# Optimization experiments

Hardware: AMD Instinct MI355X
Metric: run time of the kernel (lower is better)

Reference implementation:

```python
import jax, jax.numpy as jnp
import numpy as np
from jax import lax

NUM_CLASSES = 19
BINS_NUM = 51
LOSS_WEIGHT = 1.0


def setup_inputs() -> dict:
    key = jax.random.key(0)
    k1, k2 = jax.random.split(key)
    feature = jax.random.normal(k1, (1, 256, 64, 64), dtype=jnp.float32)
    label = jax.random.randint(k2, (1, 1, 64, 64), 0, NUM_CLASSES).astype(jnp.int64)
    return {"feature": feature, "label": label}


def reference(feature, label):
    # feature: [1, D, H, W]; label: [1, 1, H, W] (same spatial size -> nearest resize is identity)
    D = feature.shape[1]
    C = NUM_CLASSES
    F = feature[0].reshape(D, -1).T            # [N, D] pixel feature vectors
    L = label[0, 0].reshape(-1).astype(jnp.int32)  # [N] class id per pixel

    counts = jax.ops.segment_sum(jnp.ones(L.shape, jnp.float32), L, num_segments=C)  # [C]
    sum_f = jax.ops.segment_sum(F, L, num_segments=C)        # [C, D]
    sum_f2 = jax.ops.segment_sum(F * F, L, num_segments=C)   # [C, D]
    has = counts > 0
    cnt = jnp.maximum(counts, 1.0)
    miu = sum_f / cnt[:, None]                                # first-iter: direct assignment (no EMA yet)
    moment2 = sum_f2 / cnt[:, None]
    var = jnp.maximum(moment2 - miu ** 2, 1e-12)
    # stats are computed via detached numpy in the original -> no grad
    miu = lax.stop_gradient(miu)
    var = lax.stop_gradient(var)
    var_sample = var / 25.0

    bins = jnp.linspace(-5.0, 5.0, BINS_NUM).astype(jnp.float32)  # [B]

    # target gaussian pdf per (class, feature-dim, bin): [C, D, B]
    inv_norm_t = 1.0 / jnp.sqrt(2.0 * jnp.pi * var)
    target = jnp.exp(-0.5 * (bins[None, None, :] - miu[:, :, None]) ** 2 / var[:, :, None]) * inv_norm_t[:, :, None]

    # sample KDE per pixel, scatter-added into its class: [N, D, B] -> [C, D, B]
    vs_p = var_sample[L]                                      # [N, D]
    inv_norm_s = 1.0 / jnp.sqrt(2.0 * jnp.pi * vs_p)          # [N, D]
    K = jnp.exp(-0.5 * (bins[None, None, :] - F[:, :, None]) ** 2 / vs_p[:, :, None]) * inv_norm_s[:, :, None]
    samp = jax.ops.segment_sum(K, L, num_segments=C)          # [C, D, B]

    samp_den = jnp.where(has[:, None], jnp.maximum(samp.sum(-1), 1e-30), 1.0)[:, :, None]
    tgt_den = jnp.where(has[:, None], jnp.maximum(target.sum(-1), 1e-30), 1.0)[:, :, None]
    hist = samp / samp_den
    target = target / tgt_den

    # smooth L1 (beta=1, mean reduction) per class
    diff = hist - target
    ad = jnp.abs(diff)
    sl1 = jnp.where(ad < 1.0, 0.5 * diff * diff, ad - 0.5).mean(axis=(1, 2))  # [C]

    active = has & (jnp.arange(C) > 0)
    active_num = jnp.sum(active.astype(jnp.float32))
    loss = jnp.sum(jnp.where(active, sl1, 0.0)) / (active_num + 1e-12)
    return (LOSS_WEIGHT * loss, feature)
```

## Files before the change

### kernel.cpp

```cpp
#include <hip/hip_runtime.h>

#define N_PIX 4096
#define N_D   256
#define N_C   19
#define N_B   51
#define N_BLOCKS_MAIN (18 * 64)

#define OFF_LIST   0
#define OFF_COUNTS 311296
#define OFF_ACC    311424
#define OFF_TICKET 311428

__global__ __launch_bounds__(256) void k_pre(const float* __restrict__ feature,
                                             const int* __restrict__ label,
                                             float* __restrict__ out,
                                             int* __restrict__ list,
                                             int* __restrict__ counts,
                                             float* __restrict__ acc,
                                             int* __restrict__ ticket) {
    const int b = blockIdx.x;
    if (b < N_C) {
        const int c = b;
        const int w = threadIdx.x >> 6;
        const int lane = threadIdx.x & 63;
        __shared__ int wcnt[4];
        if (c == 0 && threadIdx.x == 0) { *acc = 0.f; *ticket = 0; }

        const int q0 = w * 1024;
        int cnt = 0;
        for (int base = 0; base < 1024; base += 64) {
            cnt += (int)__popcll(__ballot(label[q0 + base + lane] == c));
        }
        if (lane == 0) wcnt[w] = cnt;
        __syncthreads();
        int m = 0;
#pragma unroll
        for (int i = 0; i < 4; ++i) m += (i < w) ? wcnt[i] : 0;

        for (int base = 0; base < 1024; base += 64) {
            const int n = q0 + base + lane;
            const bool match = (label[n] == c);
            const unsigned long long mask = __ballot(match);
            if (match) list[c * N_PIX + m + __popcll(mask & ((1ull << lane) - 1ull))] = n;
            m += (int)__popcll(mask);
        }
        if (w == 3 && lane == 0) counts[c] = m;
    } else {
        const int tid = (b - N_C) * 256 + threadIdx.x;
        const int nth = (256 - N_C) * 256;
        const float4* __restrict__ src = (const float4*)feature;
        float* __restrict__ dst = out + 1;
        for (int i = tid; i < N_PIX * N_D / 4; i += nth) {
            const float4 v = src[i];
            dst[4 * i + 0] = v.x;
            dst[4 * i + 1] = v.y;
            dst[4 * i + 2] = v.z;
            dst[4 * i + 3] = v.w;
        }
    }
}

__global__ __launch_bounds__(256) void k_main(const float* __restrict__ feature,
                                              const int* __restrict__ list,
                                              const int* __restrict__ counts,
                                              float* __restrict__ acc,
                                              int* __restrict__ ticket,
                                              float* __restrict__ out) {
    const int c = blockIdx.x + 1;
    const int w = threadIdx.x >> 6;
    const int d = blockIdx.y * 4 + w;
    const int lane = threadIdx.x & 63;
    const int m = counts[c];
    __shared__ float blk[4];
    float part = 0.f;
    if (m > 0) {
        const float* __restrict__ row = feature + d * N_PIX;
        const int* __restrict__ lst = list + c * N_PIX;

        float s1 = 0.f, s2 = 0.f;
        for (int j = lane; j < m; j += 64) {
            const float f = row[lst[j]];
            s1 += f;
            s2 += f * f;
        }
#pragma unroll
        for (int off = 32; off; off >>= 1) {
            s1 += __shfl_xor(s1, off);
            s2 += __shfl_xor(s2, off);
        }
        const float cnt = (float)m;
        const float mu = s1 / cnt;
        const float v = fmaxf(s2 / cnt - mu * mu, 1e-12f);

        const float LOG2E = 1.44269504088896340736f;
        const float as = -12.5f * LOG2E / v;
        const float at = -0.5f * LOG2E / v;
        const float bin = (lane < N_B) ? fmaf(0.2f, (float)lane, -5.0f) : 1e18f;
        const float tt = bin - mu;
        const float targ = __builtin_amdgcn_exp2f(at * tt * tt);

        float a0 = 0.f, a1 = 0.f, a2 = 0.f, a3 = 0.f;
        for (int base = 0; base < m; base += 64) {
            const int j = base + lane;
            const float fl = (j < m) ? row[lst[j]] : -1e18f;
#pragma unroll
            for (int k = 0; k < 64; k += 4) {
                const float f0 = __shfl(fl, k);
                const float f1 = __shfl(fl, k + 1);
                const float f2 = __shfl(fl, k + 2);
                const float f3 = __shfl(fl, k + 3);
                const float t0 = f0 - bin, t1 = f1 - bin, t2 = f2 - bin, t3 = f3 - bin;
                a0 += __builtin_amdgcn_exp2f(as * t0 * t0);
                a1 += __builtin_amdgcn_exp2f(as * t1 * t1);
                a2 += __builtin_amdgcn_exp2f(as * t2 * t2);
                a3 += __builtin_amdgcn_exp2f(as * t3 * t3);
            }
        }
        const float acc_s = (a0 + a1) + (a2 + a3);

        float ss = acc_s, st = targ;
#pragma unroll
        for (int off = 32; off; off >>= 1) {
            ss += __shfl_xor(ss, off);
            st += __shfl_xor(st, off);
        }
        const float hist = acc_s / fmaxf(ss, 1e-30f);
        const float tgt  = targ  / fmaxf(st, 1e-30f);
        const float diff = hist - tgt;
        const float ad = fabsf(diff);
        float sl1 = (ad < 1.f) ? 0.5f * diff * diff : ad - 0.5f;
#pragma unroll
        for (int off = 32; off; off >>= 1) sl1 += __shfl_down(sl1, off);
        part = sl1;
    }
    if (lane == 0) blk[w] = part;
    __syncthreads();
    if (threadIdx.x == 0) {
        atomicAdd(acc, blk[0] + blk[1] + blk[2] + blk[3]);
        __threadfence();
        const int t = atomicAdd(ticket, 1);
        if (t == N_BLOCKS_MAIN - 1) {
            int active = 0;
            for (int cc = 1; cc < N_C; ++cc) active += (counts[cc] > 0) ? 1 : 0;
            const float total = atomicAdd(acc, 0.0f);
            out[0] = total / (float)(N_D * N_B) / ((float)active + 1e-12f);
        }
    }
}

extern "C" void kernel_launch(void* const* d_in, const int* in_sizes, int n_in,
                              void* d_out, int out_size, void* d_ws, size_t ws_size,
                              hipStream_t stream) {
    const float* feature = (const float*)d_in[0];
    const int* label = (const int*)d_in[1];
    float* out = (float*)d_out;
    char* ws = (char*)d_ws;
    int* list = (int*)(ws + OFF_LIST);
    int* counts = (int*)(ws + OFF_COUNTS);
    float* acc = (float*)(ws + OFF_ACC);
    int* ticket = (int*)(ws + OFF_TICKET);

    k_pre<<<256, 256, 0, stream>>>(feature, label, out, list, counts, acc, ticket);
    dim3 grid(N_C - 1, N_D / 4);
    k_main<<<grid, 256, 0, stream>>>(feature, list, counts, acc, ticket, out);
}
```

Before: 104.6 us.

## Map pixels to lanes with per-lane bin accumulators and cache feature loads

Changes the main loop so each lane handles its own pixel and keeps 51 per-bin accumulators in registers, in place of broadcasting each pixel to all lanes with shuffles where each lane owns one bin. This removes the per-pixel shuffles and keeps all 64 lanes busy, where the old mapping left 13 of them on dummy bins. Up to six chunks of gathered features are cached in registers so the second pass does not re-gather them. The cost is 51 cross-lane butterfly reductions at the end and higher register pressure, which may lower occupancy.

```diff
diff --git a/kernel.cpp b/kernel.cpp
--- a/kernel.cpp
+++ b/kernel.cpp
@@ -4,6 +4,7 @@
 #define N_D   256
 #define N_C   19
 #define N_B   51
+#define CACHE 6
 #define N_BLOCKS_MAIN (18 * 64)
 
 #define OFF_LIST   0
@@ -76,12 +77,17 @@
     if (m > 0) {
         const float* __restrict__ row = feature + d * N_PIX;
         const int* __restrict__ lst = list + c * N_PIX;
+        const int nch = (m + 63) >> 6;
 
+        float fc[CACHE];
         float s1 = 0.f, s2 = 0.f;
-        for (int j = lane; j < m; j += 64) {
-            const float f = row[lst[j]];
-            s1 += f;
-            s2 += f * f;
+        for (int ch = 0; ch < nch; ++ch) {
+            const int j = (ch << 6) + lane;
+            const bool valid = (j < m);
+            const float f = valid ? row[lst[j]] : -1e18f;
+            if (ch < CACHE) fc[ch] = f;
+            s1 += valid ? f : 0.f;
+            s2 += valid ? f * f : 0.f;
         }
 #pragma unroll
         for (int off = 32; off; off >>= 1) {
@@ -95,42 +101,49 @@
         const float LOG2E = 1.44269504088896340736f;
         const float as = -12.5f * LOG2E / v;
         const float at = -0.5f * LOG2E / v;
-        const float bin = (lane < N_B) ? fmaf(0.2f, (float)lane, -5.0f) : 1e18f;
-        const float tt = bin - mu;
-        const float targ = __builtin_amdgcn_exp2f(at * tt * tt);
 
-        float a0 = 0.f, a1 = 0.f, a2 = 0.f, a3 = 0.f;
-        for (int base = 0; base < m; base += 64) {
-            const int j = base + lane;
-            const float fl = (j < m) ? row[lst[j]] : -1e18f;
+        float a[N_B];
 #pragma unroll
-            for (int k = 0; k < 64; k += 4) {
-                const float f0 = __shfl(fl, k);
-                const float f1 = __shfl(fl, k + 1);
-                const float f2 = __shfl(fl, k + 2);
-                const float f3 = __shfl(fl, k + 3);
-                const float t0 = f0 - bin, t1 = f1 - bin, t2 = f2 - bin, t3 = f3 - bin;
-                a0 += __builtin_amdgcn_exp2f(as * t0 * t0);
-                a1 += __builtin_amdgcn_exp2f(as * t1 * t1);
-                a2 += __builtin_amdgcn_exp2f(as * t2 * t2);
-                a3 += __builtin_amdgcn_exp2f(as * t3 * t3);
+        for (int b = 0; b < N_B; ++b) a[b] = 0.f;
+        for (int ch = 0; ch < nch; ++ch) {
+            float f;
+            if (ch < CACHE) f = fc[ch];
+            else {
+                const int j = (ch << 6) + lane;
+                f = (j < m) ? row[lst[j]] : -1e18f;
+            }
+#pragma unroll
+            for (int b = 0; b < N_B; ++b) {
+                const float bin = -5.0f + 0.2f * (float)b;
+                const float t = f - bin;
+                a[b] += __builtin_amdgcn_exp2f(as * t * t);
             }
         }
-        const float acc_s = (a0 + a1) + (a2 + a3);
 
-        float ss = acc_s, st = targ;
 #pragma unroll
-        for (int off = 32; off; off >>= 1) {
-            ss += __shfl_xor(ss, off);
-            st += __shfl_xor(st, off);
+        for (int b = 0; b < N_B; ++b) {
+#pragma unroll
+            for (int off = 32; off; off >>= 1) a[b] += __shfl_xor(a[b], off);
         }
-        const float hist = acc_s / fmaxf(ss, 1e-30f);
-        const float tgt  = targ  / fmaxf(st, 1e-30f);
-        const float diff = hist - tgt;
-        const float ad = fabsf(diff);
-        float sl1 = (ad < 1.f) ? 0.5f * diff * diff : ad - 0.5f;
+
+        float ss = 0.f, st = 0.f;
 #pragma unroll
-        for (int off = 32; off; off >>= 1) sl1 += __shfl_down(sl1, off);
+        for (int b = 0; b < N_B; ++b) {
+            ss += a[b];
+            const float tt = (-5.0f + 0.2f * (float)b) - mu;
+            st += __builtin_amdgcn_exp2f(at * tt * tt);
+        }
+        const float is = 1.f / fmaxf(ss, 1e-30f);
+        const float it = 1.f / fmaxf(st, 1e-30f);
+        float sl1 = 0.f;
+#pragma unroll
+        for (int b = 0; b < N_B; ++b) {
+            const float tt = (-5.0f + 0.2f * (float)b) - mu;
+            const float tg = __builtin_amdgcn_exp2f(at * tt * tt) * it;
+            const float diff = a[b] * is - tg;
+            const float ad = fabsf(diff);
+            sl1 += (ad < 1.f) ? 0.5f * diff * diff : ad - 0.5f;
+        }
         part = sl1;
     }
     if (lane == 0) blk[w] = part;
```

Measured after the change: 110.6 us. 5.8% more time.

## Pre-gather class-sorted features into contiguous buffer and use uniform scalar loads in main kernel

Applied to the files above, without the earlier changes.

Adds a gather kernel that writes each feature row reordered by class into a contiguous workspace buffer. The main kernel then reads wave-uniform contiguous values, which can become scalar or broadcast loads, instead of doing an indexed gather plus cross-lane shuffles. The stats loop also becomes serial per lane without a reduction. The aim is to drop the shuffle overhead in the inner exp loop, at the cost of an extra kernel launch and about 4 MB of extra memory traffic.

```diff
diff --git a/kernel.cpp b/kernel.cpp
--- a/kernel.cpp
+++ b/kernel.cpp
@@ -10,6 +10,7 @@
 #define OFF_COUNTS 311296
 #define OFF_ACC    311424
 #define OFF_TICKET 311428
+#define OFF_GATH   524288
 
 __global__ __launch_bounds__(256) void k_pre(const float* __restrict__ feature,
                                              const int* __restrict__ label,
@@ -60,8 +61,27 @@
     }
 }
 
-__global__ __launch_bounds__(256) void k_main(const float* __restrict__ feature,
-                                              const int* __restrict__ list,
+__global__ __launch_bounds__(256) void k_gather(const float* __restrict__ feature,
+                                                const int* __restrict__ list,
+                                                const int* __restrict__ counts,
+                                                float* __restrict__ gath) {
+    const int d = blockIdx.x;
+    const int tid = threadIdx.x;
+    const float* __restrict__ row = feature + d * N_PIX;
+    float* __restrict__ outr = gath + d * N_PIX;
+    int base = 0;
+    for (int c = 0; c < N_C; ++c) {
+        const int mc = counts[c];
+        if ((c & 3) == (int)blockIdx.y) {
+            for (int j = tid; j < mc; j += 256) {
+                outr[base + j] = row[list[c * N_PIX + j]];
+            }
+        }
+        base += mc;
+    }
+}
+
+__global__ __launch_bounds__(256) void k_main(const float* __restrict__ gath,
                                               const int* __restrict__ counts,
                                               float* __restrict__ acc,
                                               int* __restrict__ ticket,
@@ -74,58 +94,59 @@
     __shared__ float blk[4];
     float part = 0.f;
     if (m > 0) {
-        const float* __restrict__ row = feature + d * N_PIX;
-        const int* __restrict__ lst = list + c * N_PIX;
+        int cs = 0;
+        for (int cc = 0; cc < c; ++cc) cs += counts[cc];
+        const float* __restrict__ gr = gath + d * N_PIX + cs;
 
-        float s1 = 0.f, s2 = 0.f;
-        for (int j = lane; j < m; j += 64) {
-            const float f = row[lst[j]];
-            s1 += f;
-            s2 += f * f;
+        float s1a = 0.f, s1b = 0.f, s2a = 0.f, s2b = 0.f;
+        int j = 0;
+        for (; j + 2 <= m; j += 2) {
+            const float f0 = gr[j], f1 = gr[j + 1];
+            s1a += f0; s2a = fmaf(f0, f0, s2a);
+            s1b += f1; s2b = fmaf(f1, f1, s2b);
         }
-#pragma unroll
-        for (int off = 32; off; off >>= 1) {
-            s1 += __shfl_xor(s1, off);
-            s2 += __shfl_xor(s2, off);
-        }
+        if (j < m) { const float f0 = gr[j]; s1a += f0; s2a = fmaf(f0, f0, s2a); }
         const float cnt = (float)m;
-        const float mu = s1 / cnt;
-        const float v = fmaxf(s2 / cnt - mu * mu, 1e-12f);
+        const float mu = (s1a + s1b) / cnt;
+        const float v = fmaxf((s2a + s2b) / cnt - mu * mu, 1e-12f);
 
         const float LOG2E = 1.44269504088896340736f;
         const float as = -12.5f * LOG2E / v;
         const float at = -0.5f * LOG2E / v;
         const float bin = (lane < N_B) ? fmaf(0.2f, (float)lane, -5.0f) : 1e18f;
+
+        float a0 = 0.f;
+        int jb = 0;
+        for (; jb + 8 <= m; jb += 8) {
+            const float f0 = gr[jb + 0], f1 = gr[jb + 1];
+            const float f2 = gr[jb + 2], f3 = gr[jb + 3];
+            const float f4 = gr[jb + 4], f5 = gr[jb + 5];
+            const float f6 = gr[jb + 6], f7 = gr[jb + 7];
+            float t;
+            t = f0 - bin; a0 += __builtin_amdgcn_exp2f(as * t * t);
+            t = f1 - bin; a0 += __builtin_amdgcn_exp2f(as * t * t);
+            t = f2 - bin; a0 += __builtin_amdgcn_exp2f(as * t * t);
+            t = f3 - bin; a0 += __builtin_amdgcn_exp2f(as * t * t);
+            t = f4 - bin; a0 += __builtin_amdgcn_exp2f(as * t * t);
+            t = f5 - bin; a0 += __builtin_amdgcn_exp2f(as * t * t);
+            t = f6 - bin; a0 += __builtin_amdgcn_exp2f(as * t * t);
+            t = f7 - bin; a0 += __builtin_amdgcn_exp2f(as * t * t);
+        }
+        for (; jb < m; ++jb) {
+            const float t = gr[jb] - bin;
+            a0 += __builtin_amdgcn_exp2f(as * t * t);
+        }
+
         const float tt = bin - mu;
         const float targ = __builtin_amdgcn_exp2f(at * tt * tt);
-
-        float a0 = 0.f, a1 = 0.f, a2 = 0.f, a3 = 0.f;
-        for (int base = 0; base < m; base += 64) {
-            const int j = base + lane;
-            const float fl = (j < m) ? row[lst[j]] : -1e18f;
-#pragma unroll
-            for (int k = 0; k < 64; k += 4) {
-                const float f0 = __shfl(fl, k);
-                const float f1 = __shfl(fl, k + 1);
-                const float f2 = __shfl(fl, k + 2);
-                const float f3 = __shfl(fl, k + 3);
-                const float t0 = f0 - bin, t1 = f1 - bin, t2 = f2 - bin, t3 = f3 - bin;
-                a0 += __builtin_amdgcn_exp2f(as * t0 * t0);
-                a1 += __builtin_amdgcn_exp2f(as * t1 * t1);
-                a2 += __builtin_amdgcn_exp2f(as * t2 * t2);
-                a3 += __builtin_amdgcn_exp2f(as * t3 * t3);
-            }
-        }
-        const float acc_s = (a0 + a1) + (a2 + a3);
-
-        float ss = acc_s, st = targ;
+        float ss = a0, st = targ;
 #pragma unroll
         for (int off = 32; off; off >>= 1) {
             ss += __shfl_xor(ss, off);
             st += __shfl_xor(st, off);
         }
-        const float hist = acc_s / fmaxf(ss, 1e-30f);
-        const float tgt  = targ  / fmaxf(st, 1e-30f);
+        const float hist = a0 / fmaxf(ss, 1e-30f);
+        const float tgt  = targ / fmaxf(st, 1e-30f);
         const float diff = hist - tgt;
         const float ad = fabsf(diff);
         float sl1 = (ad < 1.f) ? 0.5f * diff * diff : ad - 0.5f;
@@ -159,8 +180,10 @@
     int* counts = (int*)(ws + OFF_COUNTS);
     float* acc = (float*)(ws + OFF_ACC);
     int* ticket = (int*)(ws + OFF_TICKET);
+    float* gath = (float*)(ws + OFF_GATH);
 
     k_pre<<<256, 256, 0, stream>>>(feature, label, out, list, counts, acc, ticket);
+    k_gather<<<dim3(256, 4), 256, 0, stream>>>(feature, list, counts, gath);
     dim3 grid(N_C - 1, N_D / 4);
-    k_main<<<grid, 256, 0, stream>>>(feature, list, counts, acc, ticket, out);
+    k_main<<<grid, 256, 0, stream>>>(gath, counts, acc, ticket, out);
 }
```

Result: slower. 119.3 us (+14.1%).
